# Kernel tuning notes

Hardware: AMD Instinct MI355X
Metric: run time of the kernel (lower is better)

## Reference

```python
import jax, jax.numpy as jnp
import numpy as np

N_NODES = 100000
N_EDGES = 1600000
N_GRAPHS = 128
IN_FEATS = 128
OUT_FEATS = 64


def setup_inputs() -> dict:
    key = jax.random.key(0)
    k1, k2, k3, k4, k5, k6 = jax.random.split(key, 6)
    features = jax.random.normal(k1, (N_NODES, IN_FEATS), jnp.float32)
    src = jax.random.randint(k2, (N_EDGES,), 0, N_NODES, dtype=jnp.int32)
    dst = jax.random.randint(k3, (N_EDGES,), 0, N_NODES, dtype=jnp.int32)
    graph_ids = jnp.sort(jax.random.randint(k4, (N_NODES,), 0, N_GRAPHS, dtype=jnp.int32))
    # Xavier-uniform init as in DGL GraphConv
    lim1 = float(np.sqrt(6.0 / (IN_FEATS + IN_FEATS)))
    lim2 = float(np.sqrt(6.0 / (IN_FEATS + OUT_FEATS)))
    W1 = jax.random.uniform(k5, (IN_FEATS, IN_FEATS), jnp.float32, -lim1, lim1)
    W2 = jax.random.uniform(k6, (IN_FEATS, OUT_FEATS), jnp.float32, -lim2, lim2)
    b1 = jnp.zeros((IN_FEATS,), jnp.float32)
    b2 = jnp.zeros((OUT_FEATS,), jnp.float32)
    return {"features": features, "W1": W1, "b1": b1, "W2": W2, "b2": b2,
            "src": src, "dst": dst, "graph_ids": graph_ids, "num_graphs": N_GRAPHS}


def _graph_conv(x, W, b, src, dst, n_nodes):
    # DGL GraphConv, norm='both': D_dst^{-1/2} A D_src^{-1/2} X W + b
    ones = jnp.ones(src.shape, x.dtype)
    deg_out = jax.ops.segment_sum(ones, src, num_segments=n_nodes)
    deg_in = jax.ops.segment_sum(ones, dst, num_segments=n_nodes)
    norm_src = jax.lax.rsqrt(jnp.maximum(deg_out, 1.0))  # [N]
    norm_dst = jax.lax.rsqrt(jnp.maximum(deg_in, 1.0))   # [N]
    h = (x * norm_src[:, None]) @ W                       # dense transform first
    agg = jax.ops.segment_sum(h[src], dst, num_segments=n_nodes)  # spmm-style scatter-add
    return agg * norm_dst[:, None] + b


def reference(features, W1, b1, W2, b2, src, dst, graph_ids, num_graphs):
    n = features.shape[0]
    h = jax.nn.relu(_graph_conv(features, W1, b1, src, dst, n))
    h = jax.nn.relu(_graph_conv(h, W2, b2, src, dst, n))
    # dgl.mean_nodes: per-graph mean over nodes
    sums = jax.ops.segment_sum(h, graph_ids, num_segments=num_graphs)
    counts = jax.ops.segment_sum(jnp.ones((n, 1), h.dtype), graph_ids, num_segments=num_graphs)
    return sums / jnp.maximum(counts, 1.0)
```

## Files before the change

kernel.cpp:

```cpp
#include <hip/hip_runtime.h>
#include <hip/hip_bf16.h>


#define NPP_SHIFT 9
#define NPP 512
#define MAXP 256
#define NB 512

typedef __attribute__((ext_vector_type(8))) short frag8;
typedef __attribute__((ext_vector_type(4))) float f32x4;
typedef __attribute__((ext_vector_type(2))) float v2f;

__launch_bounds__(256)
__global__ void passA_count(const int* __restrict__ src, const int* __restrict__ dst,
                            int E, int P, int* __restrict__ counts_src,
                            int* __restrict__ counts_dst,
                            const int* __restrict__ gids, int N, int G,
                            int* __restrict__ gcnt) {
    __shared__ int h1[MAXP], h2[MAXP], h3[MAXP];
    int tid = threadIdx.x;
    for (int i = tid; i < MAXP; i += 256) { h1[i] = 0; h2[i] = 0; h3[i] = 0; }
    __syncthreads();
    int per_block = (E + NB - 1) / NB;
    int e0 = blockIdx.x * per_block;
    int e1 = min(e0 + per_block, E);
    for (int e = e0 + tid; e < e1; e += 256) {
        atomicAdd(&h1[src[e] >> NPP_SHIFT], 1);
        atomicAdd(&h2[dst[e] >> NPP_SHIFT], 1);
    }
    int npb = (N + NB - 1) / NB;
    int n0 = blockIdx.x * npb;
    int n1 = min(n0 + npb, N);
    for (int i = n0 + tid; i < n1; i += 256) atomicAdd(&h3[gids[i]], 1);
    __syncthreads();
    for (int i = tid; i < P; i += 256) {
        counts_src[(size_t)blockIdx.x * P + i] = h1[i];
        counts_dst[(size_t)blockIdx.x * P + i] = h2[i];
    }
    for (int i = tid; i < G; i += 256)
        if (h3[i]) atomicAdd(&gcnt[i], h3[i]);
}

__launch_bounds__(1024)
__global__ void scanB(const int* __restrict__ counts, int* __restrict__ offs,
                      int* __restrict__ ptot, int P) {
    __shared__ int s[1024];
    int tid = threadIdx.x;
    int p = blockIdx.x % P;
    int st = blockIdx.x / P;
    const int* c = counts + (size_t)st * NB * P;
    int v = (tid < NB) ? c[(size_t)tid * P + p] : 0;
    s[tid] = v;
    __syncthreads();
    for (int off = 1; off < 1024; off <<= 1) {
        int t = (tid >= off) ? s[tid - off] : 0;
        __syncthreads();
        s[tid] += t;
        __syncthreads();
    }
    if (tid < NB) offs[(size_t)st * NB * P + (size_t)tid * P + p] = s[tid] - v;
    if (tid == 1023) ptot[st * P + p] = s[1023];
}

__launch_bounds__(256)
__global__ void passC_scatter(const int* __restrict__ src, const int* __restrict__ dst,
                              int E, int P, const int* __restrict__ offs,
                              const int* __restrict__ ptot, int* __restrict__ pbase,
                              int* __restrict__ ebuf_src, int2* __restrict__ ebuf_dst) {
    __shared__ int cur1[MAXP], cur2[MAXP], sc[256];
    int tid = threadIdx.x;
    int v = (tid < P) ? ptot[tid] : 0;
    sc[tid] = v;
    __syncthreads();
    for (int off = 1; off < 256; off <<= 1) {
        int t = (tid >= off) ? sc[tid - off] : 0;
        __syncthreads();
        sc[tid] += t;
        __syncthreads();
    }
    int base0 = sc[tid] - v;
    if (tid < P) {
        cur1[tid] = base0 + offs[(size_t)blockIdx.x * P + tid];
        if (blockIdx.x == 0) pbase[tid] = base0;
    }
    __syncthreads();
    v = (tid < P) ? ptot[P + tid] : 0;
    sc[tid] = v;
    __syncthreads();
    for (int off = 1; off < 256; off <<= 1) {
        int t = (tid >= off) ? sc[tid - off] : 0;
        __syncthreads();
        sc[tid] += t;
        __syncthreads();
    }
    int base1 = sc[tid] - v;
    if (tid < P) {
        cur2[tid] = base1 + offs[(size_t)NB * P + (size_t)blockIdx.x * P + tid];
        if (blockIdx.x == 0) pbase[P + tid] = base1;
    }
    __syncthreads();
    int per_block = (E + NB - 1) / NB;
    int e0 = blockIdx.x * per_block;
    int e1 = min(e0 + per_block, E);
    for (int e = e0 + tid; e < e1; e += 256) {
        int s = src[e];
        int d = dst[e];
        int pos1 = atomicAdd(&cur1[s >> NPP_SHIFT], 1);
        ebuf_src[pos1] = s;
        int pos2 = atomicAdd(&cur2[d >> NPP_SHIFT], 1);
        ebuf_dst[pos2] = make_int2(d, s);
    }
}

__launch_bounds__(512)
__global__ void passD_build(const int* __restrict__ ebuf_src, const int2* __restrict__ ebuf_dst,
                            const int* __restrict__ ptot, const int* __restrict__ pbase,
                            float* __restrict__ norm_src, int* __restrict__ row_start,
                            int* __restrict__ csr_src, int N, int E, int P) {
    __shared__ int hs[NPP], hd[NPP], sc[NPP];
    int tid = threadIdx.x;
    int p = blockIdx.x;
    int node_lo = p << NPP_SHIFT;
    int nl = min(NPP, N - node_lo);
    hs[tid] = 0;
    hd[tid] = 0;
    __syncthreads();
    int nsrc = ptot[p];
    int base_s = pbase[p];
    for (int i = tid; i < nsrc; i += 512)
        atomicAdd(&hs[ebuf_src[base_s + i] - node_lo], 1);
    int ndst = ptot[P + p];
    int base_d = pbase[P + p];
    for (int i = tid; i < ndst; i += 512)
        atomicAdd(&hd[ebuf_dst[base_d + i].x - node_lo], 1);
    __syncthreads();
    if (tid < nl) norm_src[node_lo + tid] = rsqrtf((float)max(hs[tid], 1));
    int myh = hd[tid];
    sc[tid] = myh;
    __syncthreads();
    for (int off = 1; off < 512; off <<= 1) {
        int t = (tid >= off) ? sc[tid - off] : 0;
        __syncthreads();
        sc[tid] += t;
        __syncthreads();
    }
    int row0 = base_d + sc[tid] - myh;
    if (tid < nl) row_start[node_lo + tid] = row0;
    if (p == P - 1 && tid == 0) row_start[N] = E;
    __syncthreads();
    hd[tid] = row0;
    __syncthreads();
    for (int i = tid; i < ndst; i += 512) {
        int2 r = ebuf_dst[base_d + i];
        int pos = atomicAdd(&hd[r.x - node_lo], 1);
        csr_src[pos] = r.y;
    }
}

template <int COLS, bool BF16IN, bool PERM, bool FP8OUT>
__launch_bounds__(256)
__global__ void gemm_mfma(const void* __restrict__ xin, const float* __restrict__ w,
                          const float* __restrict__ norm,
                          void* __restrict__ out, int n) {
    constexpr int NT = COLS / 16;
    __shared__ short wlds[4 * NT * 64 * 8];
    const int tid = threadIdx.x;
    for (int i = tid; i < 128 * COLS / 4; i += 256) {
        int k = (i * 4) / COLS;
        int n0 = (i * 4) % COLS;
        float4 wv;
        if constexpr (PERM) {
            int ksrc = 64 * ((k >> 2) & 1) + 16 * (k & 3) + (k >> 3);
            wv = *reinterpret_cast<const float4*>(w + (size_t)ksrc * COLS + n0);
        } else {
            wv = reinterpret_cast<const float4*>(w)[i];
        }
        int c = k >> 5, q = (k >> 3) & 3, j = k & 7;
        float vals[4] = {wv.x, wv.y, wv.z, wv.w};
#pragma unroll
        for (int u = 0; u < 4; ++u) {
            int nn = n0 + u;
            int t = nn >> 4;
            int ln = (q << 4) | (nn & 15);
            union { __hip_bfloat16 b; short s; } cv;
            cv.b = __float2bfloat16(vals[u]);
            wlds[(((c * NT + t) << 6) | ln) * 8 + j] = cv.s;
        }
    }
    __syncthreads();

    const int lane = tid & 63;
    const int wid = tid >> 6;
    const int m = lane & 15;
    const int q = lane >> 4;
    const int ntiles = (n + 15) >> 4;
    const frag8* wfr = reinterpret_cast<const frag8*>(wlds);

    for (int wt = blockIdx.x * 4 + wid; wt < ntiles; wt += gridDim.x * 4) {
        const int row = (wt << 4) + m;
        frag8 af[4];
        if (row < n) {
            if constexpr (BF16IN) {
                const frag8* xp = reinterpret_cast<const frag8*>(
                    (const __hip_bfloat16*)xin + (size_t)row * 128);
#pragma unroll
                for (int c = 0; c < 4; ++c) af[c] = xp[c * 4 + q];
            } else {
                const float* xp = (const float*)xin + (size_t)row * 128;
                float nm = norm[row];
#pragma unroll
                for (int c = 0; c < 4; ++c) {
                    int base = c * 32 + q * 8;
                    float4 v0 = *reinterpret_cast<const float4*>(xp + base);
                    float4 v1 = *reinterpret_cast<const float4*>(xp + base + 4);
                    union { frag8 f; short s[8]; } a;
                    union { __hip_bfloat16 b; short s; } cv;
                    cv.b = __float2bfloat16(v0.x * nm); a.s[0] = cv.s;
                    cv.b = __float2bfloat16(v0.y * nm); a.s[1] = cv.s;
                    cv.b = __float2bfloat16(v0.z * nm); a.s[2] = cv.s;
                    cv.b = __float2bfloat16(v0.w * nm); a.s[3] = cv.s;
                    cv.b = __float2bfloat16(v1.x * nm); a.s[4] = cv.s;
                    cv.b = __float2bfloat16(v1.y * nm); a.s[5] = cv.s;
                    cv.b = __float2bfloat16(v1.z * nm); a.s[6] = cv.s;
                    cv.b = __float2bfloat16(v1.w * nm); a.s[7] = cv.s;
                    af[c] = a.f;
                }
            }
        } else {
#pragma unroll
            for (int c = 0; c < 4; ++c) af[c] = frag8{0, 0, 0, 0, 0, 0, 0, 0};
        }
        f32x4 acc[NT] = {};
#pragma unroll
        for (int c = 0; c < 4; ++c)
#pragma unroll
            for (int t = 0; t < NT; ++t)
                acc[t] = __builtin_amdgcn_mfma_f32_16x16x32_bf16(
                    af[c], wfr[(c * NT + t) * 64 + lane], acc[t], 0, 0, 0);
#pragma unroll
        for (int r = 0; r < 4; ++r) {
            int grow = (wt << 4) + q * 4 + r;
            if (grow < n) {
                if constexpr (FP8OUT) {
                    uint w0 = 0, w1 = 0;
                    w0 = (uint)__builtin_amdgcn_cvt_pk_fp8_f32(acc[0][r], acc[1][r], (int)w0, false);
                    w0 = (uint)__builtin_amdgcn_cvt_pk_fp8_f32(acc[2][r], acc[3][r], (int)w0, true);
                    w1 = (uint)__builtin_amdgcn_cvt_pk_fp8_f32(acc[4][r], acc[5][r], (int)w1, false);
                    w1 = (uint)__builtin_amdgcn_cvt_pk_fp8_f32(acc[6][r], acc[7][r], (int)w1, true);
                    reinterpret_cast<uint2*>(out)[(size_t)grow * 16 + m] = make_uint2(w0, w1);
                } else {
                    __hip_bfloat16* ob = reinterpret_cast<__hip_bfloat16*>(out);
#pragma unroll
                    for (int t = 0; t < NT; ++t)
                        ob[(size_t)grow * COLS + t * 16 + m] = __float2bfloat16(acc[t][r]);
                }
            }
        }
    }
}

__launch_bounds__(256)
__global__ void spmm1_kernel(const uint* __restrict__ h1,
                             const int* __restrict__ row_start,
                             const int* __restrict__ csr_src,
                             const float* __restrict__ b1,
                             const float* __restrict__ norm_src,
                             uint2* __restrict__ x2n, int n) {
    int gw = (blockIdx.x * blockDim.x + threadIdx.x) >> 6;
    int lane = threadIdx.x & 63;
    if (gw >= n) return;
    int e0 = row_start[gw];
    int e1 = row_start[gw + 1];
    int a = lane >> 5;
    int s = lane & 31;
    float acc0 = 0.f, acc1 = 0.f, acc2 = 0.f, acc3 = 0.f;
    int e = e0;
    for (; e + 16 <= e1; e += 16) {
        uint v[8];
#pragma unroll
        for (int j = 0; j < 8; ++j) {
            int cs = csr_src[e + 2 * j + a];
            v[j] = h1[(size_t)cs * 32 + s];
        }
#pragma unroll
        for (int j = 0; j < 8; ++j) {
            v2f lo = __builtin_amdgcn_cvt_pk_f32_fp8((int)v[j], false);
            v2f hi = __builtin_amdgcn_cvt_pk_f32_fp8((int)v[j], true);
            acc0 += lo[0]; acc1 += lo[1]; acc2 += hi[0]; acc3 += hi[1];
        }
    }
    if (e < e1) {
        uint v[8];
#pragma unroll
        for (int j = 0; j < 8; ++j) {
            int idx = e + 2 * j + a;
            int cidx = min(idx, e1 - 1);
            int cs = csr_src[cidx];
            uint vv = h1[(size_t)cs * 32 + s];
            v[j] = (idx < e1) ? vv : 0u;
        }
#pragma unroll
        for (int j = 0; j < 8; ++j) {
            v2f lo = __builtin_amdgcn_cvt_pk_f32_fp8((int)v[j], false);
            v2f hi = __builtin_amdgcn_cvt_pk_f32_fp8((int)v[j], true);
            acc0 += lo[0]; acc1 += lo[1]; acc2 += hi[0]; acc3 += hi[1];
        }
    }
    acc0 += __shfl_xor(acc0, 32);
    acc1 += __shfl_xor(acc1, 32);
    acc2 += __shfl_xor(acc2, 32);
    acc3 += __shfl_xor(acc3, 32);
    if (a == 0) {
        float nd = rsqrtf((float)max(e1 - e0, 1));
        float ns = norm_src[gw];
        int m2 = s >> 1;
        int a2 = (s & 1) << 6;
        float f0 = fmaxf(fmaf(acc0, nd, b1[a2 + m2]), 0.f) * ns;
        float f1 = fmaxf(fmaf(acc1, nd, b1[a2 + 16 + m2]), 0.f) * ns;
        float f2 = fmaxf(fmaf(acc2, nd, b1[a2 + 32 + m2]), 0.f) * ns;
        float f3 = fmaxf(fmaf(acc3, nd, b1[a2 + 48 + m2]), 0.f) * ns;
        union { __hip_bfloat16 b; ushort u; } c0, c1, c2, c3;
        c0.b = __float2bfloat16(f0);
        c1.b = __float2bfloat16(f1);
        c2.b = __float2bfloat16(f2);
        c3.b = __float2bfloat16(f3);
        uint w0 = (uint)c0.u | ((uint)c1.u << 16);
        uint w1 = (uint)c2.u | ((uint)c3.u << 16);
        x2n[(size_t)gw * 32 + s] = make_uint2(w0, w1);
    }
}

__launch_bounds__(256)
__global__ void spmm2_kernel(const __hip_bfloat16* __restrict__ h,
                             const int* __restrict__ row_start,
                             const int* __restrict__ csr_src,
                             const float* __restrict__ b2,
                             const int* __restrict__ gids,
                             const int* __restrict__ gcnt,
                             float* __restrict__ out, int n) {
    int gw = (blockIdx.x * blockDim.x + threadIdx.x) >> 6;
    int lane = threadIdx.x & 63;
    int wave = threadIdx.x >> 6;
    const ushort* hp = reinterpret_cast<const ushort*>(h);
    float val = 0.f;
    int g;
    if (gw < n) {
        g = gids[gw];
        int e0 = row_start[gw];
        int e1 = row_start[gw + 1];
        float acc = 0.f;
        int e = e0;
        for (; e + 16 <= e1; e += 16) {
            uint v[16];
#pragma unroll
            for (int j = 0; j < 16; ++j)
                v[j] = hp[(size_t)csr_src[e + j] * 64 + lane];
#pragma unroll
            for (int j = 0; j < 16; ++j) acc += __uint_as_float(v[j] << 16);
        }
        if (e + 8 <= e1) {
            uint v[8];
#pragma unroll
            for (int j = 0; j < 8; ++j)
                v[j] = hp[(size_t)csr_src[e + j] * 64 + lane];
#pragma unroll
            for (int j = 0; j < 8; ++j) acc += __uint_as_float(v[j] << 16);
            e += 8;
        }
        if (e + 4 <= e1) {
            uint v[4];
#pragma unroll
            for (int j = 0; j < 4; ++j)
                v[j] = hp[(size_t)csr_src[e + j] * 64 + lane];
#pragma unroll
            for (int j = 0; j < 4; ++j) acc += __uint_as_float(v[j] << 16);
            e += 4;
        }
        if (e + 2 <= e1) {
            uint v0 = hp[(size_t)csr_src[e] * 64 + lane];
            uint v1 = hp[(size_t)csr_src[e + 1] * 64 + lane];
            acc += __uint_as_float(v0 << 16);
            acc += __uint_as_float(v1 << 16);
            e += 2;
        }
        if (e < e1) {
            uint v0 = hp[(size_t)csr_src[e] * 64 + lane];
            acc += __uint_as_float(v0 << 16);
        }
        float nd = rsqrtf((float)max(e1 - e0, 1));
        val = fmaxf(fmaf(acc, nd, b2[lane]), 0.f);
        val *= 1.f / (float)max(gcnt[g], 1);
    } else {
        g = gids[n - 1];
    }
    __shared__ float sbuf[4][64];
    __shared__ int sg[4];
    sbuf[wave][lane] = val;
    if (lane == 0) sg[wave] = g;
    __syncthreads();
    if (wave == 0) {
        int g0 = sg[0], g1 = sg[1], g2 = sg[2], g3 = sg[3];
        if (g0 == g1 && g1 == g2 && g2 == g3) {
            float ssum = sbuf[0][lane] + sbuf[1][lane] + sbuf[2][lane] + sbuf[3][lane];
            atomicAdd(&out[(size_t)g0 * 64 + lane], ssum);
        } else {
            atomicAdd(&out[(size_t)g0 * 64 + lane], sbuf[0][lane]);
            atomicAdd(&out[(size_t)g1 * 64 + lane], sbuf[1][lane]);
            atomicAdd(&out[(size_t)g2 * 64 + lane], sbuf[2][lane]);
            atomicAdd(&out[(size_t)g3 * 64 + lane], sbuf[3][lane]);
        }
    }
}

extern "C" void kernel_launch(void* const* d_in, const int* in_sizes, int n_in,
                              void* d_out, int out_size, void* d_ws, size_t ws_size,
                              hipStream_t stream) {
    const float* features = (const float*)d_in[0];
    const float* W1 = (const float*)d_in[1];
    const float* b1 = (const float*)d_in[2];
    const float* W2 = (const float*)d_in[3];
    const float* b2 = (const float*)d_in[4];
    const int* src = (const int*)d_in[5];
    const int* dst = (const int*)d_in[6];
    const int* gids = (const int*)d_in[7];
    const int N = in_sizes[7];
    const int E = in_sizes[5];
    const int G = out_size / 64;
    float* out = (float*)d_out;
    const int P = (N + NPP - 1) >> NPP_SHIFT;

    char* ws = (char*)d_ws;
    size_t off = 0;
    auto alloc = [&](size_t bytes) -> void* {
        void* p = ws + off;
        off = (off + bytes + 255) & ~(size_t)255;
        return p;
    };
    int* counts = (int*)alloc((size_t)2 * NB * P * 4);
    int* offs = (int*)alloc((size_t)2 * NB * P * 4);
    int* ptot = (int*)alloc((size_t)2 * P * 4);
    int* pbase = (int*)alloc((size_t)2 * P * 4);
    int* gcnt = (int*)alloc((size_t)G * 4);
    int* ebuf_src = (int*)alloc((size_t)E * 4);
    int2* ebuf_dst = (int2*)alloc((size_t)E * 8);
    float* norm_src = (float*)alloc((size_t)N * 4);
    int* row_start = (int*)alloc((size_t)(N + 1) * 4);
    int* csr_src = (int*)alloc((size_t)E * 4);
    uint* h1 = (uint*)alloc((size_t)N * 128);
    __hip_bfloat16* x2n = (__hip_bfloat16*)alloc((size_t)N * 128 * 2);
    __hip_bfloat16* h2 = (__hip_bfloat16*)h1;

    hipMemsetAsync(out, 0, (size_t)out_size * sizeof(float), stream);
    hipMemsetAsync(gcnt, 0, (size_t)G * 4, stream);

    const int B = 256;
    passA_count<<<NB, 256, 0, stream>>>(src, dst, E, P, counts, counts + (size_t)NB * P,
                                        gids, N, G, gcnt);
    scanB<<<2 * P, 1024, 0, stream>>>(counts, offs, ptot, P);
    passC_scatter<<<NB, 256, 0, stream>>>(src, dst, E, P, offs, ptot, pbase,
                                          ebuf_src, ebuf_dst);
    passD_build<<<P, 512, 0, stream>>>(ebuf_src, ebuf_dst, ptot, pbase, norm_src, row_start,
                                       csr_src, N, E, P);

    gemm_mfma<128, false, false, true><<<768, 256, 0, stream>>>(features, W1, norm_src,
                                                                (void*)h1, N);
    spmm1_kernel<<<(N * 64 + B - 1) / B, B, 0, stream>>>(h1, row_start, csr_src, b1, norm_src,
                                                         (uint2*)x2n, N);
    gemm_mfma<64, true, true, false><<<768, 256, 0, stream>>>(x2n, W2, nullptr,
                                                              (void*)h2, N);
    spmm2_kernel<<<(N * 64 + B - 1) / B, B, 0, stream>>>(h2, row_start, csr_src, b2,
                                                         gids, gcnt, out, N);
}
```

Baseline: 305.1 us.

## Store layer-2 hidden features as FP8 and gather 4 edges per wave

The second GEMM now writes its 64-wide output as packed FP8 (64 bytes per row) instead of bf16. The layer-2 SpMM is restructured so each wave gathers four neighbor rows at once, with 16 lanes per row each loading one packed dword of four FP8 values. Partial sums are combined with cross-lane shuffles. This halves gather bandwidth and raises memory-level parallelism, at the cost of lower precision in the second layer's aggregation.

```diff
diff --git a/kernel.cpp b/kernel.cpp
--- a/kernel.cpp
+++ b/kernel.cpp
@@ -241,13 +241,18 @@
         for (int r = 0; r < 4; ++r) {
             int grow = (wt << 4) + q * 4 + r;
             if (grow < n) {
-                if constexpr (FP8OUT) {
+                if constexpr (FP8OUT && COLS == 128) {
                     uint w0 = 0, w1 = 0;
                     w0 = (uint)__builtin_amdgcn_cvt_pk_fp8_f32(acc[0][r], acc[1][r], (int)w0, false);
                     w0 = (uint)__builtin_amdgcn_cvt_pk_fp8_f32(acc[2][r], acc[3][r], (int)w0, true);
                     w1 = (uint)__builtin_amdgcn_cvt_pk_fp8_f32(acc[4][r], acc[5][r], (int)w1, false);
                     w1 = (uint)__builtin_amdgcn_cvt_pk_fp8_f32(acc[6][r], acc[7][r], (int)w1, true);
                     reinterpret_cast<uint2*>(out)[(size_t)grow * 16 + m] = make_uint2(w0, w1);
+                } else if constexpr (FP8OUT) {
+                    uint w0 = 0;
+                    w0 = (uint)__builtin_amdgcn_cvt_pk_fp8_f32(acc[0][r], acc[1][r], (int)w0, false);
+                    w0 = (uint)__builtin_amdgcn_cvt_pk_fp8_f32(acc[2][r], acc[3][r], (int)w0, true);
+                    reinterpret_cast<uint*>(out)[(size_t)grow * 16 + m] = w0;
                 } else {
                     __hip_bfloat16* ob = reinterpret_cast<__hip_bfloat16*>(out);
 #pragma unroll
@@ -331,7 +336,7 @@
 }
 
 __launch_bounds__(256)
-__global__ void spmm2_kernel(const __hip_bfloat16* __restrict__ h,
+__global__ void spmm2_kernel(const uint* __restrict__ h2,
                              const int* __restrict__ row_start,
                              const int* __restrict__ csr_src,
                              const float* __restrict__ b2,
@@ -341,61 +346,65 @@
     int gw = (blockIdx.x * blockDim.x + threadIdx.x) >> 6;
     int lane = threadIdx.x & 63;
     int wave = threadIdx.x >> 6;
-    const ushort* hp = reinterpret_cast<const ushort*>(h);
-    float val = 0.f;
+    int a = lane >> 4;
+    int s = lane & 15;
+    float f0 = 0.f, f1 = 0.f, f2 = 0.f, f3 = 0.f;
     int g;
     if (gw < n) {
         g = gids[gw];
         int e0 = row_start[gw];
         int e1 = row_start[gw + 1];
-        float acc = 0.f;
+        float v0 = 0.f, v1 = 0.f, v2 = 0.f, v3 = 0.f;
         int e = e0;
         for (; e + 16 <= e1; e += 16) {
-            uint v[16];
-#pragma unroll
-            for (int j = 0; j < 16; ++j)
-                v[j] = hp[(size_t)csr_src[e + j] * 64 + lane];
-#pragma unroll
-            for (int j = 0; j < 16; ++j) acc += __uint_as_float(v[j] << 16);
-        }
-        if (e + 8 <= e1) {
-            uint v[8];
-#pragma unroll
-            for (int j = 0; j < 8; ++j)
-                v[j] = hp[(size_t)csr_src[e + j] * 64 + lane];
-#pragma unroll
-            for (int j = 0; j < 8; ++j) acc += __uint_as_float(v[j] << 16);
-            e += 8;
-        }
-        if (e + 4 <= e1) {
-            uint v[4];
+            uint u[4];
 #pragma unroll
             for (int j = 0; j < 4; ++j)
-                v[j] = hp[(size_t)csr_src[e + j] * 64 + lane];
-#pragma unroll
-            for (int j = 0; j < 4; ++j) acc += __uint_as_float(v[j] << 16);
-            e += 4;
-        }
-        if (e + 2 <= e1) {
-            uint v0 = hp[(size_t)csr_src[e] * 64 + lane];
-            uint v1 = hp[(size_t)csr_src[e + 1] * 64 + lane];
-            acc += __uint_as_float(v0 << 16);
-            acc += __uint_as_float(v1 << 16);
-            e += 2;
+                u[j] = h2[(size_t)csr_src[e + 4 * j + a] * 16 + s];
+#pragma unroll
+            for (int j = 0; j < 4; ++j) {
+                v2f lo = __builtin_amdgcn_cvt_pk_f32_fp8((int)u[j], false);
+                v2f hi = __builtin_amdgcn_cvt_pk_f32_fp8((int)u[j], true);
+                v0 += lo[0]; v1 += lo[1]; v2 += hi[0]; v3 += hi[1];
+            }
         }
         if (e < e1) {
-            uint v0 = hp[(size_t)csr_src[e] * 64 + lane];
-            acc += __uint_as_float(v0 << 16);
-        }
+            uint u[4];
+#pragma unroll
+            for (int j = 0; j < 4; ++j) {
+                int idx = e + 4 * j + a;
+                int cidx = min(idx, e1 - 1);
+                uint vv = h2[(size_t)csr_src[cidx] * 16 + s];
+                u[j] = (idx < e1) ? vv : 0u;
+            }
+#pragma unroll
+            for (int j = 0; j < 4; ++j) {
+                v2f lo = __builtin_amdgcn_cvt_pk_f32_fp8((int)u[j], false);
+                v2f hi = __builtin_amdgcn_cvt_pk_f32_fp8((int)u[j], true);
+                v0 += lo[0]; v1 += lo[1]; v2 += hi[0]; v3 += hi[1];
+            }
+        }
+        v0 += __shfl_xor(v0, 16); v0 += __shfl_xor(v0, 32);
+        v1 += __shfl_xor(v1, 16); v1 += __shfl_xor(v1, 32);
+        v2 += __shfl_xor(v2, 16); v2 += __shfl_xor(v2, 32);
+        v3 += __shfl_xor(v3, 16); v3 += __shfl_xor(v3, 32);
         float nd = rsqrtf((float)max(e1 - e0, 1));
-        val = fmaxf(fmaf(acc, nd, b2[lane]), 0.f);
-        val *= 1.f / (float)max(gcnt[g], 1);
+        float inv = 1.f / (float)max(gcnt[g], 1);
+        f0 = fmaxf(fmaf(v0, nd, b2[s]), 0.f) * inv;
+        f1 = fmaxf(fmaf(v1, nd, b2[16 + s]), 0.f) * inv;
+        f2 = fmaxf(fmaf(v2, nd, b2[32 + s]), 0.f) * inv;
+        f3 = fmaxf(fmaf(v3, nd, b2[48 + s]), 0.f) * inv;
     } else {
         g = gids[n - 1];
     }
     __shared__ float sbuf[4][64];
     __shared__ int sg[4];
-    sbuf[wave][lane] = val;
+    if (a == 0) {
+        sbuf[wave][s] = f0;
+        sbuf[wave][16 + s] = f1;
+        sbuf[wave][32 + s] = f2;
+        sbuf[wave][48 + s] = f3;
+    }
     if (lane == 0) sg[wave] = g;
     __syncthreads();
     if (wave == 0) {
@@ -448,7 +457,7 @@
     int* csr_src = (int*)alloc((size_t)E * 4);
     uint* h1 = (uint*)alloc((size_t)N * 128);
     __hip_bfloat16* x2n = (__hip_bfloat16*)alloc((size_t)N * 128 * 2);
-    __hip_bfloat16* h2 = (__hip_bfloat16*)h1;
+    uint* h2 = h1;
 
     hipMemsetAsync(out, 0, (size_t)out_size * sizeof(float), stream);
     hipMemsetAsync(gcnt, 0, (size_t)G * 4, stream);
@@ -466,8 +475,8 @@
                                                                 (void*)h1, N);
     spmm1_kernel<<<(N * 64 + B - 1) / B, B, 0, stream>>>(h1, row_start, csr_src, b1, norm_src,
                                                          (uint2*)x2n, N);
-    gemm_mfma<64, true, true, false><<<768, 256, 0, stream>>>(x2n, W2, nullptr,
-                                                              (void*)h2, N);
+    gemm_mfma<64, true, true, true><<<768, 256, 0, stream>>>(x2n, W2, nullptr,
+                                                             (void*)h2, N);
     spmm2_kernel<<<(N * 64 + B - 1) / B, B, 0, stream>>>(h2, row_start, csr_src, b2,
                                                          gids, gcnt, out, N);
 }
```

Measured after the change: 291.0 us. 1.05x faster.
